# Kernel tuning notes

Hardware: AMD Instinct MI355X
Metric: run time of the kernel (lower is better)

The kernel has to match this reference:

```python
import jax, jax.numpy as jnp
import numpy as np

N = 4_000_000
F = 8   # EXPERIMENTS['full'] feature count
H = 16  # hidden width of both MLPs
NBINS = 28


def _lin_init(k, i, o):
    return jax.random.normal(k, (i, o), jnp.float32) * (1.0 / np.sqrt(i))


def setup_inputs() -> dict:
    key = jax.random.key(0)
    ks = jax.random.split(key, 16)
    inp = {
        "x_feat": jax.random.normal(ks[0], (N, F), jnp.float32),
        # mh MLP params
        "mh_W1": _lin_init(ks[1], F, H), "mh_b1": jnp.zeros((H,), jnp.float32),
        "mh_W2": _lin_init(ks[2], H, H), "mh_b2": jnp.zeros((H,), jnp.float32),
        "mh_W3": _lin_init(ks[3], H, 1), "mh_b3": jnp.zeros((1,), jnp.float32),
        # mh_less MLP params (input dim 1 = Size)
        "ml_W1": _lin_init(ks[4], 1, H), "ml_b1": jnp.zeros((H,), jnp.float32),
        "ml_W2": _lin_init(ks[5], H, H), "ml_b2": jnp.zeros((H,), jnp.float32),
        "ml_W3": _lin_init(ks[6], H, 1), "ml_b3": jnp.zeros((1,), jnp.float32),
    }
    # deletion sizes in 1..40 (some > 28 exercise the skip branch)
    del_lens = jax.random.randint(ks[7], (N,), 1, 41, jnp.int32)
    eq = jax.random.bernoulli(ks[8], 0.3, (N,))
    alt = jax.random.randint(ks[9], (N,), 1, 41, jnp.int32)
    inp["del_lens"] = del_lens
    inp["mh_len"] = jnp.where(eq, del_lens, alt).astype(jnp.int32)
    return inp


def _mlp(x, W1, b1, W2, b2, W3, b3):
    h = jax.nn.sigmoid(x @ W1 + b1)
    h = jax.nn.sigmoid(h @ W2 + b2)
    return h @ W3 + b3  # [N, 1]


def reference(x_feat, mh_W1, mh_b1, mh_W2, mh_b2, mh_W3, mh_b3,
              ml_W1, ml_b1, ml_W2, ml_b2, ml_W3, ml_b3,
              del_lens, mh_len):
    dl_f = del_lens.astype(x_feat.dtype)[:, None]  # [N,1]
    # psi score: exp(phi - dl*0.25)
    mh_scores = jnp.exp(_mlp(x_feat, mh_W1, mh_b1, mh_W2, mh_b2, mh_W3, mh_b3)
                        - dl_f * 0.25)[:, 0]  # [N]
    # mh_less score on Size, added only where del_len == homologyLength
    mhless = jnp.exp(_mlp(dl_f, ml_W1, ml_b1, ml_W2, ml_b2, ml_W3, ml_b3)
                     - dl_f * 0.25)[:, 0]  # [N]
    mhfull_contribution = jnp.where(del_lens == mh_len, mhless, 0.0)
    y_mh_phi = mh_scores + mhfull_contribution  # [N]

    # mh_less scores for dl = 1..28
    dls = jnp.arange(1, NBINS + 1, dtype=x_feat.dtype)[:, None]  # [28,1]
    dl2_scores = jnp.exp(_mlp(dls, ml_W1, ml_b1, ml_W2, ml_b2, ml_W3, ml_b3)
                         - dls * 0.25)[:, 0]  # [28]

    # scatter-add mh_scores into bin (dl-1), skipping dl > 28
    vals = jnp.where(del_lens <= NBINS, mh_scores, 0.0)
    seg = jnp.clip(del_lens - 1, 0, NBINS - 1)
    mh_contribution = jax.ops.segment_sum(vals, seg, num_segments=NBINS)
    y_mh_less_phi = dl2_scores + mh_contribution  # [28]

    return (y_mh_phi, y_mh_less_phi)
```

## Files before the change

kernel.cpp:

```cpp
#include <hip/hip_runtime.h>
#include <math.h>

#define NBINS 28
#define L2E 1.44269504088896340736f

#define EXP2F(x) __builtin_amdgcn_exp2f(x)
#define RCPF(x)  __builtin_amdgcn_rcpf(x)

#define WS_TBL 0
#define WS_W1  64
#define WS_B1  192
#define WS_W2  208
#define WS_B2  464
#define WS_W3  480
#define WS_B3  496
#define WS_TOT 512

__global__ void prep_kernel(const float* __restrict__ mh_W1, const float* __restrict__ mh_b1,
                            const float* __restrict__ mh_W2, const float* __restrict__ mh_b2,
                            const float* __restrict__ mh_W3, const float* __restrict__ mh_b3,
                            const float* __restrict__ ml_W1, const float* __restrict__ ml_b1,
                            const float* __restrict__ ml_W2, const float* __restrict__ ml_b2,
                            const float* __restrict__ ml_W3, const float* __restrict__ ml_b3,
                            float* __restrict__ ws, float* __restrict__ out_bins) {
    const int t = threadIdx.x;
    for (int k = t; k < 128; k += 64) ws[WS_W1 + k] = -L2E * mh_W1[k];
    for (int k = t; k < 16;  k += 64) ws[WS_B1 + k] = -L2E * mh_b1[k];
    for (int k = t; k < 256; k += 64) ws[WS_W2 + k] = -L2E * mh_W2[k];
    for (int k = t; k < 16;  k += 64) ws[WS_B2 + k] = -L2E * mh_b2[k];
    for (int k = t; k < 16;  k += 64) ws[WS_W3 + k] =  L2E * mh_W3[k];
    if (t == 0) ws[WS_B3] = L2E * mh_b3[0];

    if (t < 40) {
        const float x = (float)(t + 1);
        float h1[16], h2[16];
        #pragma unroll
        for (int j = 0; j < 16; ++j)
            h1[j] = 1.0f / (1.0f + expf(-(x * ml_W1[j] + ml_b1[j])));
        #pragma unroll
        for (int j = 0; j < 16; ++j) {
            float a = ml_b2[j];
            #pragma unroll
            for (int k = 0; k < 16; ++k) a = fmaf(h1[k], ml_W2[k * 16 + j], a);
            h2[j] = 1.0f / (1.0f + expf(-a));
        }
        float phi = ml_b3[0];
        #pragma unroll
        for (int k = 0; k < 16; ++k) phi = fmaf(h2[k], ml_W3[k], phi);
        const float sc = expf(phi - 0.25f * x);
        ws[WS_TBL + t] = sc;
        if (t < NBINS) out_bins[t] = sc;
    }
}

__global__ __launch_bounds__(256) void main_kernel(
        const float4* __restrict__ x4,
        const int4* __restrict__ dl4p,
        const int4* __restrict__ ml4p,
        const float* __restrict__ ws,
        float4* __restrict__ out4,
        float* __restrict__ out_bins,
        int nquad) {
    __shared__ float s_tbl[40];
    __shared__ float s_bins[4 * NBINS];
    const int tid = threadIdx.x;
    if (tid < 40) s_tbl[tid] = ws[WS_TBL + tid];
    if (tid < 4 * NBINS) s_bins[tid] = 0.0f;
    __syncthreads();

    const int q = blockIdx.x * 256 + tid;
    const bool active = (q < nquad);
    const int qc = active ? q : 0;

    float xf[4][8];
    #pragma unroll
    for (int r = 0; r < 4; ++r) {
        const float4 a = x4[8 * qc + 2 * r + 0];
        const float4 b = x4[8 * qc + 2 * r + 1];
        xf[r][0] = a.x; xf[r][1] = a.y; xf[r][2] = a.z; xf[r][3] = a.w;
        xf[r][4] = b.x; xf[r][5] = b.y; xf[r][6] = b.z; xf[r][7] = b.w;
    }
    const int4 dl = dl4p[qc];
    const int4 ml = ml4p[qc];
    const int dlv[4] = {dl.x, dl.y, dl.z, dl.w};
    const int mlv[4] = {ml.x, ml.y, ml.z, ml.w};

    float u[4][16];
    #pragma unroll
    for (int j = 0; j < 16; ++j) {
        const float b = ws[WS_B1 + j];
        #pragma unroll
        for (int r = 0; r < 4; ++r) u[r][j] = b;
    }
    #pragma unroll
    for (int f = 0; f < 8; ++f) {
        #pragma unroll
        for (int j = 0; j < 16; ++j) {
            const float w = ws[WS_W1 + f * 16 + j];
            #pragma unroll
            for (int r = 0; r < 4; ++r) u[r][j] = fmaf(xf[r][f], w, u[r][j]);
        }
    }
    float h[4][16];
    #pragma unroll
    for (int j = 0; j < 16; ++j) {
        #pragma unroll
        for (int r = 0; r < 4; ++r) h[r][j] = RCPF(1.0f + EXP2F(u[r][j]));
    }

    float v[4][16];
    #pragma unroll
    for (int j = 0; j < 16; ++j) {
        const float b = ws[WS_B2 + j];
        #pragma unroll
        for (int r = 0; r < 4; ++r) v[r][j] = b;
    }
    #pragma unroll
    for (int k = 0; k < 16; ++k) {
        #pragma unroll
        for (int j = 0; j < 16; ++j) {
            const float w = ws[WS_W2 + k * 16 + j];
            #pragma unroll
            for (int r = 0; r < 4; ++r) v[r][j] = fmaf(h[r][k], w, v[r][j]);
        }
    }

    const float pb = ws[WS_B3];
    float phi[4] = {pb, pb, pb, pb};
    #pragma unroll
    for (int j = 0; j < 16; ++j) {
        const float w3 = ws[WS_W3 + j];
        #pragma unroll
        for (int r = 0; r < 4; ++r)
            phi[r] = fmaf(RCPF(1.0f + EXP2F(v[r][j])), w3, phi[r]);
    }
    float sc[4];
    #pragma unroll
    for (int r = 0; r < 4; ++r)
        sc[r] = EXP2F(fmaf((float)dlv[r], -0.25f * L2E, phi[r]));

    if (active) {
        float ov[4];
        #pragma unroll
        for (int r = 0; r < 4; ++r) {
            const int i = min(max(dlv[r], 1), 40) - 1;
            ov[r] = sc[r] + ((dlv[r] == mlv[r]) ? s_tbl[i] : 0.0f);
        }
        float4 o; o.x = ov[0]; o.y = ov[1]; o.z = ov[2]; o.w = ov[3];
        out4[q] = o;
        float* myb = &s_bins[(tid >> 6) * NBINS];
        #pragma unroll
        for (int r = 0; r < 4; ++r)
            if (dlv[r] >= 1 && dlv[r] <= NBINS)
                unsafeAtomicAdd(&myb[dlv[r] - 1], sc[r]);
    }

    __syncthreads();
    if (tid < NBINS) {
        const float bsum = s_bins[tid] + s_bins[NBINS + tid] +
                           s_bins[2 * NBINS + tid] + s_bins[3 * NBINS + tid];
        unsafeAtomicAdd(&out_bins[tid], bsum);
    }
}

extern "C" void kernel_launch(void* const* d_in, const int* in_sizes, int n_in,
                              void* d_out, int out_size, void* d_ws, size_t ws_size,
                              hipStream_t stream) {
    const int n = in_sizes[0] / 8;

    const float* x_feat = (const float*)d_in[0];
    const float* mh_W1  = (const float*)d_in[1];
    const float* mh_b1  = (const float*)d_in[2];
    const float* mh_W2  = (const float*)d_in[3];
    const float* mh_b2  = (const float*)d_in[4];
    const float* mh_W3  = (const float*)d_in[5];
    const float* mh_b3  = (const float*)d_in[6];
    const float* ml_W1  = (const float*)d_in[7];
    const float* ml_b1  = (const float*)d_in[8];
    const float* ml_W2  = (const float*)d_in[9];
    const float* ml_b2  = (const float*)d_in[10];
    const float* ml_W3  = (const float*)d_in[11];
    const float* ml_b3  = (const float*)d_in[12];
    const int* del_lens = (const int*)d_in[13];
    const int* mh_len   = (const int*)d_in[14];

    float* out      = (float*)d_out;
    float* out_bins = out + n;
    float* ws       = (float*)d_ws;

    prep_kernel<<<dim3(1), dim3(64), 0, stream>>>(
        mh_W1, mh_b1, mh_W2, mh_b2, mh_W3, mh_b3,
        ml_W1, ml_b1, ml_W2, ml_b2, ml_W3, ml_b3,
        ws, out_bins);

    const int nquad = n / 4;
    const int nblocks = (nquad + 255) / 256;
    main_kernel<<<dim3(nblocks), dim3(256), 0, stream>>>(
        (const float4*)x_feat, (const int4*)del_lens, (const int4*)mh_len,
        ws, (float4*)out, out_bins, nquad);
}
```

Baseline: 305.3 us.

## Use packed fp16 dot2 for MLP layers and grid-stride loop with prefetch

Packs the first two MLP layers' weights and activations into fp16 pairs and computes them with v_dot2 (fp16 inputs, fp32 accumulate), halving the FMA instruction count in the compute-bound inner layers. The grid becomes a persistent 1024-block grid-stride loop that prefetches the next quad's inputs while the current one computes, and it does fewer block-level bin flushes. This costs precision, since inputs and hidden activations are rounded to fp16, and the prefetch buffer adds register pressure that may lower occupancy.

```diff
diff --git a/kernel.cpp b/kernel.cpp
--- a/kernel.cpp
+++ b/kernel.cpp
@@ -6,6 +6,18 @@
 
 #define EXP2F(x) __builtin_amdgcn_exp2f(x)
 #define RCPF(x)  __builtin_amdgcn_rcpf(x)
+
+typedef __fp16 h2t __attribute__((ext_vector_type(2)));
+
+static __device__ __forceinline__ float fdot2(h2t a, h2t b, float c) {
+    return __builtin_amdgcn_fdot2(a, b, c, false);
+}
+static __device__ __forceinline__ h2t pkx(float lo, float hi) {
+    return __builtin_amdgcn_cvt_pkrtz(lo, hi);
+}
+static __device__ __forceinline__ h2t asH2(float f) {
+    union { float f; h2t h; } u; u.f = f; return u.h;
+}
 
 #define WS_TBL 0
 #define WS_W1  64
@@ -14,7 +26,9 @@
 #define WS_B2  464
 #define WS_W3  480
 #define WS_B3  496
-#define WS_TOT 512
+#define WP_W1  512
+#define WP_W2  576
+#define WS_TOT 704
 
 __global__ void prep_kernel(const float* __restrict__ mh_W1, const float* __restrict__ mh_b1,
                             const float* __restrict__ mh_W2, const float* __restrict__ mh_b2,
@@ -31,6 +45,21 @@
     for (int k = t; k < 16;  k += 64) ws[WS_W3 + k] =  L2E * mh_W3[k];
     if (t == 0) ws[WS_B3] = L2E * mh_b3[0];
 
+    for (int k = t; k < 64; k += 64) {
+        const int f2 = k >> 4, j = k & 15;
+        union { __fp16 h[2]; float f; } u;
+        u.h[0] = (__fp16)(-L2E * mh_W1[(2 * f2)     * 16 + j]);
+        u.h[1] = (__fp16)(-L2E * mh_W1[(2 * f2 + 1) * 16 + j]);
+        ws[WP_W1 + k] = u.f;
+    }
+    for (int k = t; k < 128; k += 64) {
+        const int k2 = k >> 4, j = k & 15;
+        union { __fp16 h[2]; float f; } u;
+        u.h[0] = (__fp16)(-L2E * mh_W2[(2 * k2)     * 16 + j]);
+        u.h[1] = (__fp16)(-L2E * mh_W2[(2 * k2 + 1) * 16 + j]);
+        ws[WP_W2 + k] = u.f;
+    }
+
     if (t < 40) {
         const float x = (float)(t + 1);
         float h1[16], h2[16];
@@ -52,6 +81,11 @@
         if (t < NBINS) out_bins[t] = sc;
     }
 }
+
+struct QuadIn {
+    float4 x[8];
+    int4 dl, ml;
+};
 
 __global__ __launch_bounds__(256) void main_kernel(
         const float4* __restrict__ x4,
@@ -60,7 +94,7 @@
         const float* __restrict__ ws,
         float4* __restrict__ out4,
         float* __restrict__ out_bins,
-        int nquad) {
+        int nquad, int stride, int iters) {
     __shared__ float s_tbl[40];
     __shared__ float s_bins[4 * NBINS];
     const int tid = threadIdx.x;
@@ -68,91 +102,117 @@
     if (tid < 4 * NBINS) s_bins[tid] = 0.0f;
     __syncthreads();
 
-    const int q = blockIdx.x * 256 + tid;
-    const bool active = (q < nquad);
-    const int qc = active ? q : 0;
-
-    float xf[4][8];
-    #pragma unroll
-    for (int r = 0; r < 4; ++r) {
-        const float4 a = x4[8 * qc + 2 * r + 0];
-        const float4 b = x4[8 * qc + 2 * r + 1];
-        xf[r][0] = a.x; xf[r][1] = a.y; xf[r][2] = a.z; xf[r][3] = a.w;
-        xf[r][4] = b.x; xf[r][5] = b.y; xf[r][6] = b.z; xf[r][7] = b.w;
-    }
-    const int4 dl = dl4p[qc];
-    const int4 ml = ml4p[qc];
-    const int dlv[4] = {dl.x, dl.y, dl.z, dl.w};
-    const int mlv[4] = {ml.x, ml.y, ml.z, ml.w};
-
-    float u[4][16];
-    #pragma unroll
-    for (int j = 0; j < 16; ++j) {
-        const float b = ws[WS_B1 + j];
-        #pragma unroll
-        for (int r = 0; r < 4; ++r) u[r][j] = b;
-    }
-    #pragma unroll
-    for (int f = 0; f < 8; ++f) {
-        #pragma unroll
-        for (int j = 0; j < 16; ++j) {
-            const float w = ws[WS_W1 + f * 16 + j];
-            #pragma unroll
-            for (int r = 0; r < 4; ++r) u[r][j] = fmaf(xf[r][f], w, u[r][j]);
-        }
-    }
-    float h[4][16];
-    #pragma unroll
-    for (int j = 0; j < 16; ++j) {
-        #pragma unroll
-        for (int r = 0; r < 4; ++r) h[r][j] = RCPF(1.0f + EXP2F(u[r][j]));
-    }
-
-    float v[4][16];
-    #pragma unroll
-    for (int j = 0; j < 16; ++j) {
-        const float b = ws[WS_B2 + j];
-        #pragma unroll
-        for (int r = 0; r < 4; ++r) v[r][j] = b;
-    }
-    #pragma unroll
-    for (int k = 0; k < 16; ++k) {
-        #pragma unroll
-        for (int j = 0; j < 16; ++j) {
-            const float w = ws[WS_W2 + k * 16 + j];
-            #pragma unroll
-            for (int r = 0; r < 4; ++r) v[r][j] = fmaf(h[r][k], w, v[r][j]);
-        }
-    }
-
-    const float pb = ws[WS_B3];
-    float phi[4] = {pb, pb, pb, pb};
-    #pragma unroll
-    for (int j = 0; j < 16; ++j) {
-        const float w3 = ws[WS_W3 + j];
+    float* myb = &s_bins[(tid >> 6) * NBINS];
+
+    int q = blockIdx.x * 256 + tid;
+
+    QuadIn cur;
+    {
+        const int qc = (q < nquad) ? q : 0;
+        #pragma unroll
+        for (int i = 0; i < 8; ++i) cur.x[i] = x4[8 * qc + i];
+        cur.dl = dl4p[qc];  cur.ml = ml4p[qc];
+    }
+
+    #pragma unroll 1
+    for (int it = 0; it < iters; ++it) {
+        QuadIn nxt;
+        const int qn = q + stride;
+        if (it + 1 < iters) {
+            const int qcn = (qn < nquad) ? qn : 0;
+            #pragma unroll
+            for (int i = 0; i < 8; ++i) nxt.x[i] = x4[8 * qcn + i];
+            nxt.dl = dl4p[qcn];  nxt.ml = ml4p[qcn];
+        }
+
+        const bool active = (q < nquad);
+        const int dlv[4] = {cur.dl.x, cur.dl.y, cur.dl.z, cur.dl.w};
+        const int mlv[4] = {cur.ml.x, cur.ml.y, cur.ml.z, cur.ml.w};
+
+        h2t xp[4][4];
+        #pragma unroll
+        for (int r = 0; r < 4; ++r) {
+            const float4 a = cur.x[2 * r + 0];
+            const float4 b = cur.x[2 * r + 1];
+            xp[r][0] = pkx(a.x, a.y); xp[r][1] = pkx(a.z, a.w);
+            xp[r][2] = pkx(b.x, b.y); xp[r][3] = pkx(b.z, b.w);
+        }
+
+        float u[4][16];
+        #pragma unroll
+        for (int j = 0; j < 16; ++j) {
+            const float b = ws[WS_B1 + j];
+            #pragma unroll
+            for (int r = 0; r < 4; ++r) u[r][j] = b;
+        }
+        #pragma unroll
+        for (int f2 = 0; f2 < 4; ++f2) {
+            #pragma unroll
+            for (int j = 0; j < 16; ++j) {
+                const h2t w = asH2(ws[WP_W1 + f2 * 16 + j]);
+                #pragma unroll
+                for (int r = 0; r < 4; ++r) u[r][j] = fdot2(xp[r][f2], w, u[r][j]);
+            }
+        }
+        h2t hp[4][8];
+        #pragma unroll
+        for (int k2 = 0; k2 < 8; ++k2) {
+            #pragma unroll
+            for (int r = 0; r < 4; ++r) {
+                const float ha = RCPF(1.0f + EXP2F(u[r][2 * k2]));
+                const float hb = RCPF(1.0f + EXP2F(u[r][2 * k2 + 1]));
+                hp[r][k2] = pkx(ha, hb);
+            }
+        }
+
+        float v[4][16];
+        #pragma unroll
+        for (int j = 0; j < 16; ++j) {
+            const float b = ws[WS_B2 + j];
+            #pragma unroll
+            for (int r = 0; r < 4; ++r) v[r][j] = b;
+        }
+        #pragma unroll
+        for (int k2 = 0; k2 < 8; ++k2) {
+            #pragma unroll
+            for (int j = 0; j < 16; ++j) {
+                const h2t w = asH2(ws[WP_W2 + k2 * 16 + j]);
+                #pragma unroll
+                for (int r = 0; r < 4; ++r) v[r][j] = fdot2(hp[r][k2], w, v[r][j]);
+            }
+        }
+
+        const float pb = ws[WS_B3];
+        float phi[4] = {pb, pb, pb, pb};
+        #pragma unroll
+        for (int j = 0; j < 16; ++j) {
+            const float w3 = ws[WS_W3 + j];
+            #pragma unroll
+            for (int r = 0; r < 4; ++r)
+                phi[r] = fmaf(RCPF(1.0f + EXP2F(v[r][j])), w3, phi[r]);
+        }
+        float sc[4];
         #pragma unroll
         for (int r = 0; r < 4; ++r)
-            phi[r] = fmaf(RCPF(1.0f + EXP2F(v[r][j])), w3, phi[r]);
-    }
-    float sc[4];
-    #pragma unroll
-    for (int r = 0; r < 4; ++r)
-        sc[r] = EXP2F(fmaf((float)dlv[r], -0.25f * L2E, phi[r]));
-
-    if (active) {
-        float ov[4];
-        #pragma unroll
-        for (int r = 0; r < 4; ++r) {
-            const int i = min(max(dlv[r], 1), 40) - 1;
-            ov[r] = sc[r] + ((dlv[r] == mlv[r]) ? s_tbl[i] : 0.0f);
-        }
-        float4 o; o.x = ov[0]; o.y = ov[1]; o.z = ov[2]; o.w = ov[3];
-        out4[q] = o;
-        float* myb = &s_bins[(tid >> 6) * NBINS];
-        #pragma unroll
-        for (int r = 0; r < 4; ++r)
-            if (dlv[r] >= 1 && dlv[r] <= NBINS)
-                unsafeAtomicAdd(&myb[dlv[r] - 1], sc[r]);
+            sc[r] = EXP2F(fmaf((float)dlv[r], -0.25f * L2E, phi[r]));
+
+        if (active) {
+            float ov[4];
+            #pragma unroll
+            for (int r = 0; r < 4; ++r) {
+                const int i = min(max(dlv[r], 1), 40) - 1;
+                ov[r] = sc[r] + ((dlv[r] == mlv[r]) ? s_tbl[i] : 0.0f);
+            }
+            float4 o; o.x = ov[0]; o.y = ov[1]; o.z = ov[2]; o.w = ov[3];
+            out4[q] = o;
+            #pragma unroll
+            for (int r = 0; r < 4; ++r)
+                if (dlv[r] >= 1 && dlv[r] <= NBINS)
+                    unsafeAtomicAdd(&myb[dlv[r] - 1], sc[r]);
+        }
+
+        cur = nxt;
+        q = qn;
     }
 
     __syncthreads();
@@ -194,8 +254,12 @@
         ws, out_bins);
 
     const int nquad = n / 4;
-    const int nblocks = (nquad + 255) / 256;
+    int nblocks = 1024;
+    const int needed = (nquad + 255) / 256;
+    if (needed < nblocks) nblocks = needed;
+    const int stride = nblocks * 256;
+    const int iters = (nquad + stride - 1) / stride;
     main_kernel<<<dim3(nblocks), dim3(256), 0, stream>>>(
         (const float4*)x_feat, (const int4*)del_lens, (const int4*)mh_len,
-        ws, (float4*)out, out_bins, nquad);
-}
+        ws, (float4*)out, out_bins, nquad, stride, iters);
+}
```

After: 274.3 us. 1.11x faster.
